# Performance work log

Hardware: AMD Instinct MI355X
Metric: run time of the kernel (lower is better)

Reference implementation:

```python
import jax, jax.numpy as jnp
import numpy as np

DIM = 256
RES = 64
HEADS = 8
WS = 8            # window_size
CS = (8, 64)      # cross_size (cs1 == W so cross grid broadcasts against window grid)
HEAD_DIM = DIM // HEADS
SCALE = HEAD_DIM ** -0.5


def _partition(x, B, sh, sw):
    # x: [B, L, C] -> [B*heads, H//sh, W//sw, sh*sw, head_dim]
    H = W = RES
    C = DIM
    x = x.reshape(B, H // sh, sh, W // sw, sw, HEADS, HEAD_DIM)
    x = x.transpose(0, 5, 1, 3, 2, 4, 6)
    return x.reshape(B * HEADS, H // sh, W // sw, sh * sw, HEAD_DIM)


def setup_inputs() -> dict:
    key = jax.random.key(0)
    qkv = jax.random.normal(key, (3, 8, RES * RES, DIM), dtype=jnp.float32)
    return {"qkv": qkv}


def reference(qkv) -> jnp.ndarray:
    q, k, v = qkv[0], qkv[1], qkv[2]
    B, L, C = q.shape
    H = W = RES

    qw = _partition(q, B, WS, WS) * SCALE            # [Bh, H/ws, W/ws, ws*ws, hd]
    kc = _partition(k, B, CS[0], CS[1])              # [Bh, H/cs0, 1, cs0*cs1, hd]
    vc = _partition(v, B, CS[0], CS[1])

    # Original einsum 'bhwnc,bqkmc->bhwnm' sums k over its cross-window grid (q,k axes);
    # equivalently pre-sum k over those axes, then contract over head_dim.
    k_sum = kc.sum(axis=(1, 2))                      # [Bh, m, hd]
    attn = jnp.einsum('bhwnc,bmc->bhwnm', qw, k_sum) # [Bh, H/ws, W/ws, n, m]
    attn = jax.nn.softmax(attn, axis=-1)

    # broadcast matmul: vc's cross grid (H/cs0, 1) broadcasts to (H/ws, W/ws)
    x = attn @ vc                                    # [Bh, H/ws, W/ws, n, hd]

    x = x.reshape(B, HEADS, H // WS, W // WS, WS, WS, HEAD_DIM)
    x = x.transpose(0, 2, 4, 3, 5, 1, 6).reshape(B, H, W, C).reshape(B, -1, C)
    return x
```

## Files before the change

kernel.cpp:

```cpp
#include <hip/hip_runtime.h>
#include <hip/hip_bf16.h>

#define NB 8
#define L_TOT 4096
#define DIM 256
#define HEADS 8
#define HEAD_DIM 32
#define M_TOT 512
#define QSCALE (0.17677669529663687f * 1.4426950408889634f)

typedef float f32x16 __attribute__((ext_vector_type(16)));
typedef short bf16x8 __attribute__((ext_vector_type(8)));

union BF8 { bf16x8 v; unsigned u[4]; uint2 u2[2]; };

__device__ __forceinline__ unsigned cvt2(float lo, float hi) {
    __hip_bfloat162 h = __float22bfloat162_rn(make_float2(lo, hi));
    union { __hip_bfloat162 h2; unsigned u; } un;
    un.h2 = h;
    return un.u;
}

__global__ __launch_bounds__(256) void ksum_kernel(const float* __restrict__ k,
                                                   unsigned short* __restrict__ ks) {
    const int blk = blockIdx.x;
    const int bh = blk >> 4, part = blk & 15;
    const int b = bh >> 3, head = bh & 7;
    const float* kb = k + (size_t)b * L_TOT * DIM + head * HEAD_DIM;
    const int c0 = (threadIdx.x & 7) * 4;
    const int m = part * 32 + (threadIdx.x >> 3);
    float4 s = make_float4(0.f, 0.f, 0.f, 0.f);
#pragma unroll
    for (int hq = 0; hq < 8; ++hq) {
        const float4 f = *(const float4*)(kb + (size_t)(hq * 512 + m) * DIM + c0);
        s.x += f.x; s.y += f.y; s.z += f.z; s.w += f.w;
    }
    uint2 o;
    o.x = cvt2(s.x, s.y);
    o.y = cvt2(s.z, s.w);
    *(uint2*)(ks + ((size_t)bh * M_TOT + m) * HEAD_DIM + c0) = o;
}

template <bool USE_WS>
__global__ __launch_bounds__(512, 8) void attn_kernel(const float* __restrict__ q,
                                                      const float* __restrict__ kg,
                                                      const float* __restrict__ v,
                                                      const unsigned short* __restrict__ ks,
                                                      float* __restrict__ out) {
    __shared__ unsigned short smem[USE_WS ? (32 * 516) : (32 * 516 + 512 * 36)];
    unsigned short* vT = smem;

    const int tid = threadIdx.x;
    const int wave = tid >> 6;
    const int lane = tid & 63;
    const int ql = lane & 31;
    const int hi = lane >> 5;

    const int bid = blockIdx.x;
    const int wk = (bid & 7) * 128 + (bid >> 3);
    const int bh = wk >> 4, h = (wk >> 1) & 7, half = wk & 1;
    const int b = bh >> 3, head = bh & 7;

    const float* vbase = v + ((size_t)b * L_TOT + h * M_TOT) * DIM + head * HEAD_DIM;

#pragma unroll
    for (int it = 0; it < 8; ++it) {
        const int idx = it * 512 + tid;
        const int m = idx >> 3, c0 = (idx & 7) * 4;
        const float4 f = *(const float4*)(vbase + (size_t)m * DIM + c0);
        const unsigned w0 = cvt2(f.x, f.y), w1 = cvt2(f.z, f.w);
        vT[(c0 + 0) * 516 + m] = (unsigned short)w0;
        vT[(c0 + 1) * 516 + m] = (unsigned short)(w0 >> 16);
        vT[(c0 + 2) * 516 + m] = (unsigned short)w1;
        vT[(c0 + 3) * 516 + m] = (unsigned short)(w1 >> 16);
    }
    unsigned short* KS = smem + 32 * 516;
    if (!USE_WS) {
        const float* kb = kg + (size_t)b * L_TOT * DIM + head * HEAD_DIM;
        for (int idx = tid; idx < M_TOT * HEAD_DIM; idx += 512) {
            const int m = idx >> 5, c = idx & 31;
            float s = 0.f;
#pragma unroll
            for (int hq = 0; hq < 8; ++hq)
                s += kb[(size_t)(hq * 512 + m) * DIM + c];
            KS[m * 36 + c] = (unsigned short)cvt2(s, 0.f);
        }
    }
    __syncthreads();

    const int g = half * 8 + wave;
    const int wcol = g >> 1, n0 = (g & 1) * 32;
    const int n = n0 + ql;
    const int Lq = (h * 8 + (n >> 3)) * 64 + wcol * 8 + (n & 7);
    const float* qp = q + ((size_t)b * L_TOT + Lq) * DIM + head * HEAD_DIM;

    BF8 qf0, qf1;
    {
        const float4 f0 = *(const float4*)(qp + 8 * hi);
        const float4 f1 = *(const float4*)(qp + 8 * hi + 4);
        qf0.u[0] = cvt2(f0.x * QSCALE, f0.y * QSCALE);
        qf0.u[1] = cvt2(f0.z * QSCALE, f0.w * QSCALE);
        qf0.u[2] = cvt2(f1.x * QSCALE, f1.y * QSCALE);
        qf0.u[3] = cvt2(f1.z * QSCALE, f1.w * QSCALE);
        const float4 f2 = *(const float4*)(qp + 16 + 8 * hi);
        const float4 f3 = *(const float4*)(qp + 16 + 8 * hi + 4);
        qf1.u[0] = cvt2(f2.x * QSCALE, f2.y * QSCALE);
        qf1.u[1] = cvt2(f2.z * QSCALE, f2.w * QSCALE);
        qf1.u[2] = cvt2(f3.x * QSCALE, f3.y * QSCALE);
        qf1.u[3] = cvt2(f3.z * QSCALE, f3.w * QSCALE);
    }

    const unsigned short* ksb = ks + (size_t)bh * M_TOT * HEAD_DIM;

    f32x16 O;
#pragma unroll
    for (int r = 0; r < 16; ++r) O[r] = 0.f;
    float lsum = 0.f;

    for (int ch = 0; ch < 16; ++ch) {
        const int M0 = ch << 5;
        f32x16 S;
#pragma unroll
        for (int r = 0; r < 16; ++r) S[r] = 0.f;

        BF8 A0, A1;
        if (USE_WS) {
            A0.v = *(const bf16x8*)(ksb + (size_t)(M0 + ql) * 32 + 8 * hi);
            A1.v = *(const bf16x8*)(ksb + (size_t)(M0 + ql) * 32 + 16 + 8 * hi);
        } else {
            const unsigned short* kr = KS + (M0 + ql) * 36 + 8 * hi;
            A0.u2[0] = *(const uint2*)(kr);
            A0.u2[1] = *(const uint2*)(kr + 4);
            A1.u2[0] = *(const uint2*)(kr + 16);
            A1.u2[1] = *(const uint2*)(kr + 20);
        }
        S = __builtin_amdgcn_mfma_f32_32x32x16_bf16(A0.v, qf0.v, S, 0, 0, 0);
        S = __builtin_amdgcn_mfma_f32_32x32x16_bf16(A1.v, qf1.v, S, 0, 0, 0);

        float p[16];
#pragma unroll
        for (int r = 0; r < 16; ++r) p[r] = __builtin_amdgcn_exp2f(S[r]);
#pragma unroll
        for (int r = 0; r < 16; ++r) lsum += p[r];

        unsigned w0 = cvt2(p[0], p[1]),   w1 = cvt2(p[2], p[3]);
        unsigned w2 = cvt2(p[4], p[5]),   w3 = cvt2(p[6], p[7]);
        unsigned w4 = cvt2(p[8], p[9]),   w5 = cvt2(p[10], p[11]);
        unsigned w6 = cvt2(p[12], p[13]), w7 = cvt2(p[14], p[15]);
        asm("v_permlane32_swap_b32 %0, %1" : "+v"(w0), "+v"(w2));
        asm("v_permlane32_swap_b32 %0, %1" : "+v"(w1), "+v"(w3));
        asm("v_permlane32_swap_b32 %0, %1" : "+v"(w4), "+v"(w6));
        asm("v_permlane32_swap_b32 %0, %1" : "+v"(w5), "+v"(w7));
        BF8 PA0, PA1, VB0, VB1;
        PA0.u[0] = w0; PA0.u[1] = w1; PA0.u[2] = w2; PA0.u[3] = w3;
        PA1.u[0] = w4; PA1.u[1] = w5; PA1.u[2] = w6; PA1.u[3] = w7;
        const unsigned short* vb = vT + ql * 516 + M0 + 8 * hi;
        VB0.u2[0] = *(const uint2*)(vb);
        VB0.u2[1] = *(const uint2*)(vb + 4);
        VB1.u2[0] = *(const uint2*)(vb + 16);
        VB1.u2[1] = *(const uint2*)(vb + 20);
        O = __builtin_amdgcn_mfma_f32_32x32x16_bf16(PA0.v, VB0.v, O, 0, 0, 0);
        O = __builtin_amdgcn_mfma_f32_32x32x16_bf16(PA1.v, VB1.v, O, 0, 0, 0);
    }

    lsum += __shfl_xor(lsum, 32, 64);
    const float inv = __builtin_amdgcn_rcpf(lsum);

    const int rowBase = h * 512 + (n0 >> 3) * 64 + wcol * 8 + 4 * hi;
    float* ob = out + ((size_t)b * L_TOT + rowBase) * DIM + head * HEAD_DIM + ql;
#pragma unroll
    for (int r = 0; r < 16; ++r) {
        const float iv = __shfl(inv, (r & 3) + 8 * (r >> 2) + 4 * hi, 64);
        ob[(size_t)((r >> 2) * 64 + (r & 3)) * DIM] = O[r] * iv;
    }
}

extern "C" void kernel_launch(void* const* d_in, const int* in_sizes, int n_in,
                              void* d_out, int out_size, void* d_ws, size_t ws_size,
                              hipStream_t stream) {
    const float* qkv = (const float*)d_in[0];
    const float* q = qkv;
    const float* k = qkv + (size_t)NB * L_TOT * DIM;
    const float* v = qkv + (size_t)2 * NB * L_TOT * DIM;
    float* out = (float*)d_out;
    const size_t ks_bytes = (size_t)NB * HEADS * M_TOT * HEAD_DIM * 2;
    if (ws_size >= ks_bytes) {
        unsigned short* ks = (unsigned short*)d_ws;
        ksum_kernel<<<dim3(1024), dim3(256), 0, stream>>>(k, ks);
        attn_kernel<true><<<dim3(1024), dim3(512), 0, stream>>>(q, k, v, ks, out);
    } else {
        attn_kernel<false><<<dim3(1024), dim3(512), 0, stream>>>(q, k, v, nullptr, out);
    }
}
```

Baseline: 178.5 us.

## Software-pipeline ksum loads, hoist V reads, and use LDS for normalization

The main loop is unrolled by two with ping-pong register buffers, so the next chunk's k-sum fragments are loaded from global memory while the current chunk is computed. V fragment LDS reads are moved ahead of the exp/convert work, and the per-row reciprocal sums go through a small LDS array read as float4 instead of 16 shuffles. The occupancy hint drops from 8 to 4 blocks per unit to allow more registers. The extra registers and lower occupancy could offset the gain from hiding latency.

```diff
diff --git a/kernel.cpp b/kernel.cpp
--- a/kernel.cpp
+++ b/kernel.cpp
@@ -42,12 +42,14 @@
 }
 
 template <bool USE_WS>
-__global__ __launch_bounds__(512, 8) void attn_kernel(const float* __restrict__ q,
+__global__ __launch_bounds__(512, 4) void attn_kernel(const float* __restrict__ q,
                                                       const float* __restrict__ kg,
                                                       const float* __restrict__ v,
                                                       const unsigned short* __restrict__ ks,
                                                       float* __restrict__ out) {
-    __shared__ unsigned short smem[USE_WS ? (32 * 516) : (32 * 516 + 512 * 36)];
+    constexpr int VT_SH = 32 * 516;
+    constexpr int INV_SH = 8 * 32 * 2;
+    __shared__ unsigned short smem[USE_WS ? (VT_SH + INV_SH) : (VT_SH + INV_SH + 512 * 36)];
     unsigned short* vT = smem;
 
     const int tid = threadIdx.x;
@@ -74,7 +76,7 @@
         vT[(c0 + 2) * 516 + m] = (unsigned short)w1;
         vT[(c0 + 3) * 516 + m] = (unsigned short)(w1 >> 16);
     }
-    unsigned short* KS = smem + 32 * 516;
+    unsigned short* KS = smem + VT_SH + INV_SH;
     if (!USE_WS) {
         const float* kb = kg + (size_t)b * L_TOT * DIM + head * HEAD_DIM;
         for (int idx = tid; idx < M_TOT * HEAD_DIM; idx += 512) {
@@ -110,32 +112,44 @@
         qf1.u[3] = cvt2(f3.z * QSCALE, f3.w * QSCALE);
     }
 
-    const unsigned short* ksb = ks + (size_t)bh * M_TOT * HEAD_DIM;
+    const unsigned short* ksb = ks + (size_t)bh * (M_TOT * HEAD_DIM);
+    const unsigned short* vb0 = vT + ql * 516 + 8 * hi;
+    float* invW = (float*)(smem + VT_SH) + wave * 32;
 
     f32x16 O;
 #pragma unroll
     for (int r = 0; r < 16; ++r) O[r] = 0.f;
     float lsum = 0.f;
 
-    for (int ch = 0; ch < 16; ++ch) {
-        const int M0 = ch << 5;
-        f32x16 S;
-#pragma unroll
-        for (int r = 0; r < 16; ++r) S[r] = 0.f;
-
-        BF8 A0, A1;
+    BF8 a0, a1, b0, b1;
+    if (USE_WS) {
+        a0.v = *(const bf16x8*)(ksb + (size_t)ql * 32 + 8 * hi);
+        a1.v = *(const bf16x8*)(ksb + (size_t)ql * 32 + 16 + 8 * hi);
+    }
+
+    auto body = [&](int M0, BF8& c0, BF8& c1, BF8& p0, BF8& p1, int M0n) {
         if (USE_WS) {
-            A0.v = *(const bf16x8*)(ksb + (size_t)(M0 + ql) * 32 + 8 * hi);
-            A1.v = *(const bf16x8*)(ksb + (size_t)(M0 + ql) * 32 + 16 + 8 * hi);
+            p0.v = *(const bf16x8*)(ksb + (size_t)(M0n + ql) * 32 + 8 * hi);
+            p1.v = *(const bf16x8*)(ksb + (size_t)(M0n + ql) * 32 + 16 + 8 * hi);
         } else {
             const unsigned short* kr = KS + (M0 + ql) * 36 + 8 * hi;
-            A0.u2[0] = *(const uint2*)(kr);
-            A0.u2[1] = *(const uint2*)(kr + 4);
-            A1.u2[0] = *(const uint2*)(kr + 16);
-            A1.u2[1] = *(const uint2*)(kr + 20);
+            c0.u2[0] = *(const uint2*)(kr);
+            c0.u2[1] = *(const uint2*)(kr + 4);
+            c1.u2[0] = *(const uint2*)(kr + 16);
+            c1.u2[1] = *(const uint2*)(kr + 20);
         }
-        S = __builtin_amdgcn_mfma_f32_32x32x16_bf16(A0.v, qf0.v, S, 0, 0, 0);
-        S = __builtin_amdgcn_mfma_f32_32x32x16_bf16(A1.v, qf1.v, S, 0, 0, 0);
+        f32x16 S;
+#pragma unroll
+        for (int r = 0; r < 16; ++r) S[r] = 0.f;
+        S = __builtin_amdgcn_mfma_f32_32x32x16_bf16(c0.v, qf0.v, S, 0, 0, 0);
+        S = __builtin_amdgcn_mfma_f32_32x32x16_bf16(c1.v, qf1.v, S, 0, 0, 0);
+
+        BF8 VB0, VB1;
+        const unsigned short* vb = vb0 + M0;
+        VB0.u2[0] = *(const uint2*)(vb);
+        VB0.u2[1] = *(const uint2*)(vb + 4);
+        VB1.u2[0] = *(const uint2*)(vb + 16);
+        VB1.u2[1] = *(const uint2*)(vb + 20);
 
         float p[16];
 #pragma unroll
@@ -151,27 +165,32 @@
         asm("v_permlane32_swap_b32 %0, %1" : "+v"(w1), "+v"(w3));
         asm("v_permlane32_swap_b32 %0, %1" : "+v"(w4), "+v"(w6));
         asm("v_permlane32_swap_b32 %0, %1" : "+v"(w5), "+v"(w7));
-        BF8 PA0, PA1, VB0, VB1;
+        BF8 PA0, PA1;
         PA0.u[0] = w0; PA0.u[1] = w1; PA0.u[2] = w2; PA0.u[3] = w3;
         PA1.u[0] = w4; PA1.u[1] = w5; PA1.u[2] = w6; PA1.u[3] = w7;
-        const unsigned short* vb = vT + ql * 516 + M0 + 8 * hi;
-        VB0.u2[0] = *(const uint2*)(vb);
-        VB0.u2[1] = *(const uint2*)(vb + 4);
-        VB1.u2[0] = *(const uint2*)(vb + 16);
-        VB1.u2[1] = *(const uint2*)(vb + 20);
         O = __builtin_amdgcn_mfma_f32_32x32x16_bf16(PA0.v, VB0.v, O, 0, 0, 0);
         O = __builtin_amdgcn_mfma_f32_32x32x16_bf16(PA1.v, VB1.v, O, 0, 0, 0);
+    };
+
+    for (int i = 0; i < 8; ++i) {
+        const int M0 = i * 64;
+        body(M0,      a0, a1, b0, b1, M0 + 32);
+        body(M0 + 32, b0, b1, a0, a1, (M0 + 64) & 511);
     }
 
     lsum += __shfl_xor(lsum, 32, 64);
     const float inv = __builtin_amdgcn_rcpf(lsum);
+    if (hi == 0) invW[ql] = inv;
 
     const int rowBase = h * 512 + (n0 >> 3) * 64 + wcol * 8 + 4 * hi;
     float* ob = out + ((size_t)b * L_TOT + rowBase) * DIM + head * HEAD_DIM + ql;
 #pragma unroll
-    for (int r = 0; r < 16; ++r) {
-        const float iv = __shfl(inv, (r & 3) + 8 * (r >> 2) + 4 * hi, 64);
-        ob[(size_t)((r >> 2) * 64 + (r & 3)) * DIM] = O[r] * iv;
+    for (int t = 0; t < 4; ++t) {
+        const float4 iv = *(const float4*)(invW + 8 * t + 4 * hi);
+        ob[(size_t)(t * 64 + 0) * DIM] = O[4 * t + 0] * iv.x;
+        ob[(size_t)(t * 64 + 1) * DIM] = O[4 * t + 1] * iv.y;
+        ob[(size_t)(t * 64 + 2) * DIM] = O[4 * t + 2] * iv.z;
+        ob[(size_t)(t * 64 + 3) * DIM] = O[4 * t + 3] * iv.w;
     }
 }
 
```

Result: no change. 175.0 us (-1.9%).
